# Kernel tuning notes

Measured on AMD Instinct MI355X. Metric: run time of the kernel, lower is better.

Reference implementation:

```python
import jax, jax.numpy as jnp
import numpy as np

B, A, IN, H, NA = 256, 32, 512, 512, 64


def setup_inputs() -> dict:
    key = jax.random.key(0)
    ks = jax.random.split(key, 9)
    s = 1.0 / np.sqrt(H).astype(np.float32)
    si = 1.0 / np.sqrt(IN).astype(np.float32)
    return {
        "inputs": jax.random.normal(ks[0], (B * A, IN), jnp.float32),
        "hidden_state": jnp.zeros((B, A, H), jnp.float32),
        "W1": jax.random.normal(ks[1], (A, H, IN), jnp.float32) * si,
        "b1": jax.random.normal(ks[2], (A, H), jnp.float32) * si,
        "W_ih": jax.random.normal(ks[3], (A, 3 * H, H), jnp.float32) * s,
        "b_ih": jax.random.normal(ks[4], (A, 3 * H), jnp.float32) * s,
        "W_hh": jax.random.normal(ks[5], (A, 3 * H, H), jnp.float32) * s,
        "b_hh": jax.random.normal(ks[6], (A, 3 * H), jnp.float32) * s,
        "W2": jax.random.normal(ks[7], (A, NA, H), jnp.float32) * s,
        "b2": jax.random.normal(ks[8], (A, NA), jnp.float32) * s,
    }


def reference(inputs, hidden_state, W1, b1, W_ih, b_ih, W_hh, b_hh, W2, b2):
    # inputs: [B*A, IN] -> [B, A, IN]; per-agent distinct weights stacked on axis 0 (a)
    x = inputs.reshape(-1, A, IN)
    h_in = hidden_state  # [B, A, H]
    # fc1 + relu, grouped over agents
    x1 = jax.nn.relu(jnp.einsum('bai,ahi->bah', x, W1) + b1)
    # GRUCell (PyTorch gate layout: r, z, n)
    gx = jnp.einsum('bah,agh->bag', x1, W_ih) + b_ih   # [B, A, 3H]
    gh = jnp.einsum('bah,agh->bag', h_in, W_hh) + b_hh  # [B, A, 3H]
    gx_r, gx_z, gx_n = jnp.split(gx, 3, axis=-1)
    gh_r, gh_z, gh_n = jnp.split(gh, 3, axis=-1)
    r = jax.nn.sigmoid(gx_r + gh_r)
    z = jax.nn.sigmoid(gx_z + gh_z)
    n = jnp.tanh(gx_n + r * gh_n)
    h = (1.0 - z) * n + z * h_in  # [B, A, H]
    # fc2 per agent
    q = jnp.einsum('bah,anh->ban', h, W2) + b2  # [B, A, NA]
    # torch: cat(qs, dim=-1).view(-1, n_actions) == reshape to [B*A, NA]
    return q.reshape(-1, NA), h
```

## Files before the change

### kernel.cpp

```cpp
#include <hip/hip_runtime.h>
#include <hip/hip_bf16.h>


typedef __attribute__((ext_vector_type(8))) __bf16 bf16x8;
typedef __attribute__((ext_vector_type(4))) float  f32x4;

constexpr int NAGENT = 32;
constexpr int KC     = 512;

__device__ __forceinline__ bf16x8 cvt8(const float* p) {
  f32x4 u = *(const f32x4*)p;
  f32x4 v = *(const f32x4*)(p + 4);
  bf16x8 w;
  w[0] = (__bf16)u[0]; w[1] = (__bf16)u[1]; w[2] = (__bf16)u[2]; w[3] = (__bf16)u[3];
  w[4] = (__bf16)v[0]; w[5] = (__bf16)v[1]; w[6] = (__bf16)v[2]; w[7] = (__bf16)v[3];
  return w;
}
__device__ __forceinline__ float sigmoid_f(float x) { return 1.f / (1.f + __expf(-x)); }
__device__ __forceinline__ float tanh_f(float x) {
  float xc = fminf(fmaxf(x, -15.f), 15.f);
  float a = __expf(2.f * xc);
  return (a - 1.f) / (a + 1.f);
}
__device__ __forceinline__ int xcd_swz(int bid, int nwg) {
  return (bid & 7) * (nwg >> 3) + (bid >> 3);
}


__global__ __launch_bounds__(256) void prep_k(
    const float* __restrict__ hidden, __bf16* __restrict__ AF) {
  const int idx = blockIdx.x * 256 + threadIdx.x;
  const int kc = idx & 63;
  const int row = idx >> 6;
  const int a = row & 31, b = row >> 5;
  bf16x8 v = cvt8(hidden + (size_t)row * KC + kc * 8);
  *(bf16x8*)(AF + ((size_t)(a * 128 + 64 + kc) * 256 + b) * 8) = v;
}

__global__ __launch_bounds__(512, 2) void fc1_k(
    const float* __restrict__ inputs, const float* __restrict__ W1,
    const float* __restrict__ b1, __bf16* __restrict__ AF) {
  const int wg = xcd_swz(blockIdx.x, gridDim.x);
  const int a  = wg >> 3;
  const int n0 = (wg & 7) * 64;

  __shared__ __attribute__((aligned(16))) __bf16 lA[2][256][8][8];
  __shared__ __attribute__((aligned(16))) __bf16 lB[2][64][8][8];

  const int tid = threadIdx.x;
  const int lane = tid & 63;
  const int wave = tid >> 6;
  const int wm = wave >> 1, wn = wave & 1;
  const int lr = lane & 15, lk = lane >> 4;

  int arow[4], aks[4]; size_t aoff[4];
#pragma unroll
  for (int c = 0; c < 4; ++c) {
    const int idx = c * 512 + tid;
    arow[c] = idx >> 3; aks[c] = idx & 7;
    aoff[c] = ((size_t)arow[c] * NAGENT + a) * KC + aks[c] * 8;
  }
  const int brow = tid >> 3, bks = tid & 7;
  const size_t boff = ((size_t)a * 512 + n0 + brow) * KC + bks * 8;

  bf16x8 sA[4], sB;
  auto loadT = [&](int t) {
    const int kb = t * 64;
#pragma unroll
    for (int c = 0; c < 4; ++c) sA[c] = cvt8(inputs + aoff[c] + kb);
    sB = cvt8(W1 + boff + kb);
  };
  auto writeT = [&](int buf) {
#pragma unroll
    for (int c = 0; c < 4; ++c)
      *(bf16x8*)(&lA[buf][arow[c]][aks[c] ^ (arow[c] & 7)][0]) = sA[c];
    *(bf16x8*)(&lB[buf][brow][bks ^ (brow & 7)][0]) = sB;
  };

  f32x4 acc[4][2] = {};
  auto computeT = [&](int buf) {
#pragma unroll
    for (int s = 0; s < 2; ++s) {
      const int ks = s * 4 + lk;
      bf16x8 af[4];
#pragma unroll
      for (int i = 0; i < 4; ++i) {
        const int row = wm * 64 + i * 16 + lr;
        af[i] = *(const bf16x8*)(&lA[buf][row][ks ^ (row & 7)][0]);
      }
#pragma unroll
      for (int cb = 0; cb < 2; ++cb) {
        const int br = wn * 32 + cb * 16 + lr;
        bf16x8 bv = *(const bf16x8*)(&lB[buf][br][ks ^ (br & 7)][0]);
#pragma unroll
        for (int i = 0; i < 4; ++i)
          acc[i][cb] = __builtin_amdgcn_mfma_f32_16x16x32_bf16(af[i], bv, acc[i][cb], 0, 0, 0);
      }
    }
  };

  loadT(0); writeT(0);
  int cur = 0;
#pragma unroll 1
  for (int t = 0; t < 8; ++t) {
    __syncthreads();
    if (t < 7) loadT(t + 1);
    computeT(cur);
    if (t < 7) { writeT(cur ^ 1); cur ^= 1; }
  }

#pragma unroll
  for (int cb = 0; cb < 2; ++cb) {
    const int col = n0 + wn * 32 + cb * 16 + lr;
    const int kc = col >> 3, c7 = col & 7;
    const float bias = b1[(size_t)a * 512 + col];
#pragma unroll
    for (int i = 0; i < 4; ++i) {
      const int r0 = wm * 64 + i * 16 + lk * 4;
#pragma unroll
      for (int e = 0; e < 4; ++e) {
        const float v = fmaxf(acc[i][cb][e] + bias, 0.f);
        AF[((size_t)(a * 128 + kc) * 256 + r0 + e) * 8 + c7] = (__bf16)v;
      }
    }
  }
}

__global__ __launch_bounds__(1024, 4) void gru_k(
    const __bf16* __restrict__ AF,
    const float* __restrict__ Wih, const float* __restrict__ bih,
    const float* __restrict__ Whh, const float* __restrict__ bhh,
    float* __restrict__ hout, __bf16* __restrict__ hbf) {
  const int wg = xcd_swz(blockIdx.x, gridDim.x);
  const int a  = wg >> 3;
  const int n0 = (wg & 7) * 64;

  __shared__ __attribute__((aligned(16))) float lBf[3][192][64];

  const int tid = threadIdx.x;
  const int lane = tid & 63;
  const int wave = tid >> 6;
  const int w4 = wave * 4;
  const int wm = wave >> 1;
  const int wc = wave & 1;
  const int lr = lane & 15, lk = lane >> 4;

  int boffB[3];
#pragma unroll
  for (int c = 0; c < 3; ++c) {
    const int row = c * 64 + w4 + (lane >> 4);
    const int s2 = (lane & 15) >> 1, h = lane & 1;
    const int slot = s2 ^ (row & 7);
    boffB[c] = (a * 1536 + (row >> 6) * 512 + n0 + (row & 63)) * KC + slot * 8 + h * 4;
  }

  const int aBase = a * 262144 + lk * 2048 + (wm * 32 + lr) * 8;

  auto glB = [&](int tt, int buf) {
    const float* W = (tt < 8) ? Wih : Whh;
    const int kb = (tt & 7) * 64;
#pragma unroll
    for (int c = 0; c < 3; ++c)
      __builtin_amdgcn_global_load_lds(
          (const __attribute__((address_space(1))) unsigned*)(const void*)(W + boffB[c] + kb),
          (__attribute__((address_space(3))) unsigned*)(void*)&lBf[buf][c * 64 + w4][0],
          16, 0, 0);
  };

  auto bfrag = [&](const float* base, int row, int ks) -> bf16x8 {
    const float* p = base + row * 64 + ((ks ^ (row & 7)) << 3);
    f32x4 lo = *(const f32x4*)p;
    f32x4 hi = *(const f32x4*)(p + 4);
    bf16x8 w;
    w[0] = (__bf16)lo[0]; w[1] = (__bf16)lo[1]; w[2] = (__bf16)lo[2]; w[3] = (__bf16)lo[3];
    w[4] = (__bf16)hi[0]; w[5] = (__bf16)hi[1]; w[6] = (__bf16)hi[2]; w[7] = (__bf16)hi[3];
    return w;
  };

  f32x4 accR[2][2] = {}, accZ[2][2] = {}, accXN[2][2] = {}, accHN[2][2] = {};

  auto step = [&](int t, f32x4 (&accN)[2][2]) {
    bf16x8 af[2][2];
#pragma unroll
    for (int s = 0; s < 2; ++s)
#pragma unroll
      for (int i = 0; i < 2; ++i)
        af[s][i] = *(const bf16x8*)(AF + aBase + t * 16384 + s * 8192 + i * 128);
    __builtin_amdgcn_sched_barrier(0);
    if (t + 2 < 16) glB(t + 2, (t + 2) % 3);
    const float* base = &lBf[t % 3][0][0];
#pragma unroll
    for (int s = 0; s < 2; ++s) {
      const int ks = s * 4 + lk;
#pragma unroll
      for (int cc = 0; cc < 2; ++cc) {
        const int rr = wc * 32 + cc * 16 + lr;
        bf16x8 bR = bfrag(base, rr, ks);
        bf16x8 bZ = bfrag(base, 64 + rr, ks);
        bf16x8 bN = bfrag(base, 128 + rr, ks);
#pragma unroll
        for (int i = 0; i < 2; ++i) {
          accR[i][cc] = __builtin_amdgcn_mfma_f32_16x16x32_bf16(af[s][i], bR, accR[i][cc], 0, 0, 0);
          accZ[i][cc] = __builtin_amdgcn_mfma_f32_16x16x32_bf16(af[s][i], bZ, accZ[i][cc], 0, 0, 0);
          accN[i][cc] = __builtin_amdgcn_mfma_f32_16x16x32_bf16(af[s][i], bN, accN[i][cc], 0, 0, 0);
        }
      }
    }
    asm volatile("s_waitcnt vmcnt(3)" ::: "memory");
    __builtin_amdgcn_s_barrier();
    __builtin_amdgcn_sched_barrier(0);
  };

  glB(0, 0);
  glB(1, 1);
  asm volatile("s_waitcnt vmcnt(3)" ::: "memory");
  __builtin_amdgcn_s_barrier();
  __builtin_amdgcn_sched_barrier(0);

#pragma unroll
  for (int t = 0; t < 8; ++t) step(t, accXN);
#pragma unroll
  for (int t = 8; t < 16; ++t) step(t, accHN);

#pragma unroll
  for (int cc = 0; cc < 2; ++cc) {
    const int col = n0 + wc * 32 + cc * 16 + lr;
    const size_t ab = (size_t)a * 1536 + col;
    const float br_ = bih[ab] + bhh[ab];
    const float bz_ = bih[ab + 512] + bhh[ab + 512];
    const float bxn = bih[ab + 1024];
    const float bhn = bhh[ab + 1024];
    const size_t hfb = ((size_t)(a * 128 + 64 + (col >> 3)) * 256) * 8 + (col & 7);
#pragma unroll
    for (int i = 0; i < 2; ++i) {
      const int r0 = wm * 32 + i * 16 + lk * 4;
#pragma unroll
      for (int e = 0; e < 4; ++e) {
        const float hprev = (float)AF[hfb + (size_t)(r0 + e) * 8];
        const float r = sigmoid_f(accR[i][cc][e] + br_);
        const float z = sigmoid_f(accZ[i][cc][e] + bz_);
        const float n = tanh_f((accXN[i][cc][e] + bxn) + r * (accHN[i][cc][e] + bhn));
        const float h = (1.f - z) * n + z * hprev;
        const size_t o = ((size_t)(r0 + e) * NAGENT + a) * KC + col;
        hout[o] = h;
        hbf[o] = (__bf16)h;
      }
    }
  }
}

template <bool ABF16, int ACT, bool OBF16>
__global__ __launch_bounds__(256) void gemm64(
    const void* __restrict__ Ap, const float* __restrict__ Wp,
    const float* __restrict__ bp, void* __restrict__ Op, const int N) {
  constexpr int BM = 64, MT = 4;
  const int NT = N >> 6;
  const int wg = xcd_swz(blockIdx.x, gridDim.x);
  const int a  = wg / (MT * NT);
  const int rem = wg % (MT * NT);
  const int n0 = (rem / MT) * 64;
  const int b0 = (rem % MT) * BM;

  __shared__ __attribute__((aligned(16))) __bf16 lA[2][4][64][8];
  __shared__ __attribute__((aligned(16))) __bf16 lB[2][4][64][8];

  const int tid = threadIdx.x;
  const int lane = tid & 63;
  const int wn = tid >> 6;
  const int lr = lane & 15, lk = lane >> 4;

  const int ar = tid >> 2, aks = tid & 3;
  const size_t aoff = ((size_t)(b0 + ar) * NAGENT + a) * KC + aks * 8;
  const size_t boff = ((size_t)a * N + n0 + ar) * KC + aks * 8;

  const float*  Af = (const float*)Ap;
  const __bf16* Ab = (const __bf16*)Ap;

  bf16x8 sA, sB;
  auto loadT = [&](int t) {
    if constexpr (ABF16) sA = *(const bf16x8*)(Ab + aoff + t * 32);
    else                 sA = cvt8(Af + aoff + t * 32);
    sB = cvt8(Wp + boff + t * 32);
  };
  auto writeT = [&](int buf) {
    *(bf16x8*)(&lA[buf][aks][ar][0]) = sA;
    *(bf16x8*)(&lB[buf][aks][ar][0]) = sB;
  };

  f32x4 acc[4] = {};
  auto computeT = [&](int buf) {
    bf16x8 bv = *(const bf16x8*)(&lB[buf][lk][wn * 16 + lr][0]);
#pragma unroll
    for (int i = 0; i < 4; ++i) {
      bf16x8 af = *(const bf16x8*)(&lA[buf][lk][i * 16 + lr][0]);
      acc[i] = __builtin_amdgcn_mfma_f32_16x16x32_bf16(af, bv, acc[i], 0, 0, 0);
    }
  };

  loadT(0); writeT(0);
  int cur = 0;
#pragma unroll 1
  for (int t = 0; t < KC / 32; ++t) {
    __syncthreads();
    if (t + 1 < KC / 32) loadT(t + 1);
    computeT(cur);
    if (t + 1 < KC / 32) { writeT(cur ^ 1); cur ^= 1; }
  }

  const int col = n0 + wn * 16 + lr;
  const float bias = bp[(size_t)a * N + col];
#pragma unroll
  for (int i = 0; i < 4; ++i) {
    const int r0 = b0 + i * 16 + lk * 4;
#pragma unroll
    for (int e = 0; e < 4; ++e) {
      float v = acc[i][e] + bias;
      if (ACT == 1) v = fmaxf(v, 0.f);
      const size_t o = ((size_t)(r0 + e) * NAGENT + a) * N + col;
      if constexpr (OBF16) ((__bf16*)Op)[o] = (__bf16)v;
      else                 ((float*)Op)[o]  = v;
    }
  }
}

extern "C" void kernel_launch(void* const* d_in, const int* in_sizes, int n_in,
                              void* d_out, int out_size, void* d_ws, size_t ws_size,
                              hipStream_t stream) {
  const float* inputs = (const float*)d_in[0];
  const float* hidden = (const float*)d_in[1];
  const float* W1   = (const float*)d_in[2];
  const float* b1   = (const float*)d_in[3];
  const float* W_ih = (const float*)d_in[4];
  const float* b_ih = (const float*)d_in[5];
  const float* W_hh = (const float*)d_in[6];
  const float* b_hh = (const float*)d_in[7];
  const float* W2   = (const float*)d_in[8];
  const float* b2   = (const float*)d_in[9];

  float* out_q = (float*)d_out;
  float* out_h = out_q + (size_t)8192 * 64;

  char* ws = (char*)d_ws;
  __bf16* AF  = (__bf16*)(ws);
  __bf16* hbf = (__bf16*)(ws + ((size_t)16 << 20));

  prep_k<<<2048, 256, 0, stream>>>(hidden, AF);
  fc1_k<<<256, 512, 0, stream>>>(inputs, W1, b1, AF);
  gru_k<<<256, 1024, 0, stream>>>(AF, W_ih, b_ih, W_hh, b_hh, out_h, hbf);
  gemm64<true, 0, false><<<128, 256, 0, stream>>>(hbf, W2, b2, out_q, 64);
}
```

Measured before the change: 111.9 us.

## Stage GRU activations through LDS and switch weights to double-buffered pipeline

Measured after the change: 114.0 us. No clear change (+1.9%).

```diff
diff --git a/kernel.cpp b/kernel.cpp
--- a/kernel.cpp
+++ b/kernel.cpp
@@ -135,7 +135,8 @@
   const int a  = wg >> 3;
   const int n0 = (wg & 7) * 64;
 
-  __shared__ __attribute__((aligned(16))) float lBf[3][192][64];
+  __shared__ __attribute__((aligned(16))) float  lBf[2][192][64];
+  __shared__ __attribute__((aligned(16))) __bf16 lAb[2][16384];
 
   const int tid = threadIdx.x;
   const int lane = tid & 63;
@@ -148,13 +149,12 @@
   int boffB[3];
 #pragma unroll
   for (int c = 0; c < 3; ++c) {
-    const int row = c * 64 + w4 + (lane >> 4);
-    const int s2 = (lane & 15) >> 1, h = lane & 1;
-    const int slot = s2 ^ (row & 7);
-    boffB[c] = (a * 1536 + (row >> 6) * 512 + n0 + (row & 63)) * KC + slot * 8 + h * 4;
-  }
-
-  const int aBase = a * 262144 + lk * 2048 + (wm * 32 + lr) * 8;
+    const int r = c * 64 + w4 + (lane >> 4);
+    const int v = ((r & 7) << 1) | ((r >> 3) & 1);
+    const int q = (lane & 15) ^ v;
+    boffB[c] = (a * 1536 + (r >> 6) * 512 + n0 + (r & 63)) * KC + q * 4;
+  }
+  const int aSrc = a * 262144 + wave * 1024 + lane * 8;
 
   auto glB = [&](int tt, int buf) {
     const float* W = (tt < 8) ? Wih : Whh;
@@ -166,11 +166,21 @@
           (__attribute__((address_space(3))) unsigned*)(void*)&lBf[buf][c * 64 + w4][0],
           16, 0, 0);
   };
-
-  auto bfrag = [&](const float* base, int row, int ks) -> bf16x8 {
-    const float* p = base + row * 64 + ((ks ^ (row & 7)) << 3);
-    f32x4 lo = *(const f32x4*)p;
-    f32x4 hi = *(const f32x4*)(p + 4);
+  auto glA = [&](int t, int buf) {
+#pragma unroll
+    for (int c = 0; c < 2; ++c)
+      __builtin_amdgcn_global_load_lds(
+          (const __attribute__((address_space(1))) unsigned*)(const void*)(AF + aSrc + t * 16384 + c * 512),
+          (__attribute__((address_space(3))) unsigned*)(void*)&lAb[buf][wave * 1024 + c * 512],
+          16, 0, 0);
+  };
+
+  auto bfrag = [&](int buf, int row, int ks) -> bf16x8 {
+    const int v = ((row & 7) << 1) | ((row >> 3) & 1);
+    const float* plo = &lBf[buf][row][(((ks << 1)) ^ v) << 2];
+    const float* phi = &lBf[buf][row][(((ks << 1) | 1) ^ v) << 2];
+    f32x4 lo = *(const f32x4*)plo;
+    f32x4 hi = *(const f32x4*)phi;
     bf16x8 w;
     w[0] = (__bf16)lo[0]; w[1] = (__bf16)lo[1]; w[2] = (__bf16)lo[2]; w[3] = (__bf16)lo[3];
     w[4] = (__bf16)hi[0]; w[5] = (__bf16)hi[1]; w[6] = (__bf16)hi[2]; w[7] = (__bf16)hi[3];
@@ -179,25 +189,24 @@
 
   f32x4 accR[2][2] = {}, accZ[2][2] = {}, accXN[2][2] = {}, accHN[2][2] = {};
 
-  auto step = [&](int t, f32x4 (&accN)[2][2]) {
+  auto step = [&](int t, int buf, f32x4 (&accN)[2][2]) {
+    if (t + 1 < 16) { glA(t + 1, buf ^ 1); glB(t + 1, buf ^ 1); }
+    __builtin_amdgcn_sched_barrier(0);
     bf16x8 af[2][2];
 #pragma unroll
     for (int s = 0; s < 2; ++s)
 #pragma unroll
       for (int i = 0; i < 2; ++i)
-        af[s][i] = *(const bf16x8*)(AF + aBase + t * 16384 + s * 8192 + i * 128);
-    __builtin_amdgcn_sched_barrier(0);
-    if (t + 2 < 16) glB(t + 2, (t + 2) % 3);
-    const float* base = &lBf[t % 3][0][0];
+        af[s][i] = *(const bf16x8*)(&lAb[buf][((s * 4 + lk) * 256 + wm * 32 + i * 16 + lr) * 8]);
 #pragma unroll
     for (int s = 0; s < 2; ++s) {
       const int ks = s * 4 + lk;
 #pragma unroll
       for (int cc = 0; cc < 2; ++cc) {
         const int rr = wc * 32 + cc * 16 + lr;
-        bf16x8 bR = bfrag(base, rr, ks);
-        bf16x8 bZ = bfrag(base, 64 + rr, ks);
-        bf16x8 bN = bfrag(base, 128 + rr, ks);
+        bf16x8 bR = bfrag(buf, rr, ks);
+        bf16x8 bZ = bfrag(buf, 64 + rr, ks);
+        bf16x8 bN = bfrag(buf, 128 + rr, ks);
 #pragma unroll
         for (int i = 0; i < 2; ++i) {
           accR[i][cc] = __builtin_amdgcn_mfma_f32_16x16x32_bf16(af[s][i], bR, accR[i][cc], 0, 0, 0);
@@ -206,21 +215,20 @@
         }
       }
     }
-    asm volatile("s_waitcnt vmcnt(3)" ::: "memory");
+    asm volatile("s_waitcnt vmcnt(0)" ::: "memory");
     __builtin_amdgcn_s_barrier();
     __builtin_amdgcn_sched_barrier(0);
   };
 
-  glB(0, 0);
-  glB(1, 1);
-  asm volatile("s_waitcnt vmcnt(3)" ::: "memory");
+  glA(0, 0); glB(0, 0);
+  asm volatile("s_waitcnt vmcnt(0)" ::: "memory");
   __builtin_amdgcn_s_barrier();
   __builtin_amdgcn_sched_barrier(0);
 
 #pragma unroll
-  for (int t = 0; t < 8; ++t) step(t, accXN);
-#pragma unroll
-  for (int t = 8; t < 16; ++t) step(t, accHN);
+  for (int t = 0; t < 8; ++t) step(t, t & 1, accXN);
+#pragma unroll
+  for (int t = 8; t < 16; ++t) step(t, t & 1, accHN);
 
 #pragma unroll
   for (int cc = 0; cc < 2; ++cc) {
```

## Retile GRU kernel to 16-column blocks with 256 threads and double buffering

Applied to the files above, without the earlier changes.

Result: slower. 128.6 us (+15.0%).

```diff
diff --git a/kernel.cpp b/kernel.cpp
--- a/kernel.cpp
+++ b/kernel.cpp
@@ -126,35 +126,32 @@
   }
 }
 
-__global__ __launch_bounds__(1024, 4) void gru_k(
+__global__ __launch_bounds__(256, 3) void gru_k(
     const __bf16* __restrict__ AF,
     const float* __restrict__ Wih, const float* __restrict__ bih,
     const float* __restrict__ Whh, const float* __restrict__ bhh,
     float* __restrict__ hout, __bf16* __restrict__ hbf) {
   const int wg = xcd_swz(blockIdx.x, gridDim.x);
-  const int a  = wg >> 3;
-  const int n0 = (wg & 7) * 64;
-
-  __shared__ __attribute__((aligned(16))) float lBf[3][192][64];
+  const int a  = wg >> 5;
+  const int n0 = (wg & 31) * 16;
+
+  __shared__ __attribute__((aligned(16))) float lBf[2][48][64];
 
   const int tid = threadIdx.x;
   const int lane = tid & 63;
   const int wave = tid >> 6;
   const int w4 = wave * 4;
-  const int wm = wave >> 1;
-  const int wc = wave & 1;
   const int lr = lane & 15, lk = lane >> 4;
 
   int boffB[3];
 #pragma unroll
   for (int c = 0; c < 3; ++c) {
-    const int row = c * 64 + w4 + (lane >> 4);
-    const int s2 = (lane & 15) >> 1, h = lane & 1;
-    const int slot = s2 ^ (row & 7);
-    boffB[c] = (a * 1536 + (row >> 6) * 512 + n0 + (row & 63)) * KC + slot * 8 + h * 4;
-  }
-
-  const int aBase = a * 262144 + lk * 2048 + (wm * 32 + lr) * 8;
+    const int r = c * 16 + w4 + (lane >> 4);
+    const int v = ((r & 7) << 1) | ((r >> 3) & 1);
+    const int q = (lane & 15) ^ v;
+    boffB[c] = (a * 1536 + (r >> 4) * 512 + n0 + (r & 15)) * KC + q * 4;
+  }
+  const int aOff = a * 262144 + lk * 2048 + wave * 512 + lr * 8;
 
   auto glB = [&](int tt, int buf) {
     const float* W = (tt < 8) ? Wih : Whh;
@@ -163,88 +160,79 @@
     for (int c = 0; c < 3; ++c)
       __builtin_amdgcn_global_load_lds(
           (const __attribute__((address_space(1))) unsigned*)(const void*)(W + boffB[c] + kb),
-          (__attribute__((address_space(3))) unsigned*)(void*)&lBf[buf][c * 64 + w4][0],
+          (__attribute__((address_space(3))) unsigned*)(void*)&lBf[buf][c * 16 + w4][0],
           16, 0, 0);
   };
 
-  auto bfrag = [&](const float* base, int row, int ks) -> bf16x8 {
-    const float* p = base + row * 64 + ((ks ^ (row & 7)) << 3);
-    f32x4 lo = *(const f32x4*)p;
-    f32x4 hi = *(const f32x4*)(p + 4);
+  auto bfrag = [&](int buf, int r, int ks) -> bf16x8 {
+    const int v = ((r & 7) << 1) | ((r >> 3) & 1);
+    f32x4 lo = *(const f32x4*)&lBf[buf][r][(((ks << 1)) ^ v) << 2];
+    f32x4 hi = *(const f32x4*)&lBf[buf][r][(((ks << 1) | 1) ^ v) << 2];
     bf16x8 w;
     w[0] = (__bf16)lo[0]; w[1] = (__bf16)lo[1]; w[2] = (__bf16)lo[2]; w[3] = (__bf16)lo[3];
     w[4] = (__bf16)hi[0]; w[5] = (__bf16)hi[1]; w[6] = (__bf16)hi[2]; w[7] = (__bf16)hi[3];
     return w;
   };
 
-  f32x4 accR[2][2] = {}, accZ[2][2] = {}, accXN[2][2] = {}, accHN[2][2] = {};
-
-  auto step = [&](int t, f32x4 (&accN)[2][2]) {
-    bf16x8 af[2][2];
+  f32x4 accR[4] = {}, accZ[4] = {}, accXN[4] = {}, accHN[4] = {};
+
+  auto step = [&](int t, int buf, f32x4 (&accN)[4]) {
+    if (t + 1 < 16) glB(t + 1, buf ^ 1);
+    __builtin_amdgcn_sched_barrier(0);
+    bf16x8 af[2][4];
 #pragma unroll
     for (int s = 0; s < 2; ++s)
 #pragma unroll
-      for (int i = 0; i < 2; ++i)
-        af[s][i] = *(const bf16x8*)(AF + aBase + t * 16384 + s * 8192 + i * 128);
-    __builtin_amdgcn_sched_barrier(0);
-    if (t + 2 < 16) glB(t + 2, (t + 2) % 3);
-    const float* base = &lBf[t % 3][0][0];
+      for (int i = 0; i < 4; ++i)
+        af[s][i] = *(const bf16x8*)(AF + aOff + t * 16384 + s * 8192 + i * 128);
 #pragma unroll
     for (int s = 0; s < 2; ++s) {
       const int ks = s * 4 + lk;
-#pragma unroll
-      for (int cc = 0; cc < 2; ++cc) {
-        const int rr = wc * 32 + cc * 16 + lr;
-        bf16x8 bR = bfrag(base, rr, ks);
-        bf16x8 bZ = bfrag(base, 64 + rr, ks);
-        bf16x8 bN = bfrag(base, 128 + rr, ks);
-#pragma unroll
-        for (int i = 0; i < 2; ++i) {
-          accR[i][cc] = __builtin_amdgcn_mfma_f32_16x16x32_bf16(af[s][i], bR, accR[i][cc], 0, 0, 0);
-          accZ[i][cc] = __builtin_amdgcn_mfma_f32_16x16x32_bf16(af[s][i], bZ, accZ[i][cc], 0, 0, 0);
-          accN[i][cc] = __builtin_amdgcn_mfma_f32_16x16x32_bf16(af[s][i], bN, accN[i][cc], 0, 0, 0);
-        }
+      bf16x8 bR = bfrag(buf, lr, ks);
+      bf16x8 bZ = bfrag(buf, 16 + lr, ks);
+      bf16x8 bN = bfrag(buf, 32 + lr, ks);
+#pragma unroll
+      for (int i = 0; i < 4; ++i) {
+        accR[i] = __builtin_amdgcn_mfma_f32_16x16x32_bf16(af[s][i], bR, accR[i], 0, 0, 0);
+        accZ[i] = __builtin_amdgcn_mfma_f32_16x16x32_bf16(af[s][i], bZ, accZ[i], 0, 0, 0);
+        accN[i] = __builtin_amdgcn_mfma_f32_16x16x32_bf16(af[s][i], bN, accN[i], 0, 0, 0);
       }
     }
-    asm volatile("s_waitcnt vmcnt(3)" ::: "memory");
+    asm volatile("s_waitcnt vmcnt(0) lgkmcnt(0)" ::: "memory");
     __builtin_amdgcn_s_barrier();
     __builtin_amdgcn_sched_barrier(0);
   };
 
   glB(0, 0);
-  glB(1, 1);
-  asm volatile("s_waitcnt vmcnt(3)" ::: "memory");
+  asm volatile("s_waitcnt vmcnt(0)" ::: "memory");
   __builtin_amdgcn_s_barrier();
   __builtin_amdgcn_sched_barrier(0);
 
 #pragma unroll
-  for (int t = 0; t < 8; ++t) step(t, accXN);
-#pragma unroll
-  for (int t = 8; t < 16; ++t) step(t, accHN);
-
-#pragma unroll
-  for (int cc = 0; cc < 2; ++cc) {
-    const int col = n0 + wc * 32 + cc * 16 + lr;
-    const size_t ab = (size_t)a * 1536 + col;
-    const float br_ = bih[ab] + bhh[ab];
-    const float bz_ = bih[ab + 512] + bhh[ab + 512];
-    const float bxn = bih[ab + 1024];
-    const float bhn = bhh[ab + 1024];
-    const size_t hfb = ((size_t)(a * 128 + 64 + (col >> 3)) * 256) * 8 + (col & 7);
-#pragma unroll
-    for (int i = 0; i < 2; ++i) {
-      const int r0 = wm * 32 + i * 16 + lk * 4;
-#pragma unroll
-      for (int e = 0; e < 4; ++e) {
-        const float hprev = (float)AF[hfb + (size_t)(r0 + e) * 8];
-        const float r = sigmoid_f(accR[i][cc][e] + br_);
-        const float z = sigmoid_f(accZ[i][cc][e] + bz_);
-        const float n = tanh_f((accXN[i][cc][e] + bxn) + r * (accHN[i][cc][e] + bhn));
-        const float h = (1.f - z) * n + z * hprev;
-        const size_t o = ((size_t)(r0 + e) * NAGENT + a) * KC + col;
-        hout[o] = h;
-        hbf[o] = (__bf16)h;
-      }
+  for (int t = 0; t < 8; ++t) step(t, t & 1, accXN);
+#pragma unroll
+  for (int t = 8; t < 16; ++t) step(t, t & 1, accHN);
+
+  const int col = n0 + lr;
+  const size_t ab = (size_t)a * 1536 + col;
+  const float br_ = bih[ab] + bhh[ab];
+  const float bz_ = bih[ab + 512] + bhh[ab + 512];
+  const float bxn = bih[ab + 1024];
+  const float bhn = bhh[ab + 1024];
+  const size_t hfb = ((size_t)(a * 128 + 64 + (col >> 3)) * 256) * 8 + (col & 7);
+#pragma unroll
+  for (int i = 0; i < 4; ++i) {
+    const int r0 = wave * 64 + i * 16 + lk * 4;
+#pragma unroll
+    for (int e = 0; e < 4; ++e) {
+      const float hprev = (float)AF[hfb + (size_t)(r0 + e) * 8];
+      const float r = sigmoid_f(accR[i][e] + br_);
+      const float z = sigmoid_f(accZ[i][e] + bz_);
+      const float n = tanh_f((accXN[i][e] + bxn) + r * (accHN[i][e] + bhn));
+      const float h = (1.f - z) * n + z * hprev;
+      const size_t o = ((size_t)(r0 + e) * NAGENT + a) * KC + col;
+      hout[o] = h;
+      hbf[o] = (__bf16)h;
     }
   }
 }
@@ -346,6 +334,6 @@
 
   prep_k<<<2048, 256, 0, stream>>>(hidden, AF);
   fc1_k<<<256, 512, 0, stream>>>(inputs, W1, b1, AF);
-  gru_k<<<256, 1024, 0, stream>>>(AF, W_ih, b_ih, W_hh, b_hh, out_h, hbf);
+  gru_k<<<1024, 256, 0, stream>>>(AF, W_ih, b_ih, W_hh, b_hh, out_h, hbf);
   gemm64<true, 0, false><<<128, 256, 0, stream>>>(hbf, W2, b2, out_q, 64);
 }
```
